# Performance work log

Hardware: AMD Instinct MI355X
Metric: run time of the kernel (lower is better)

Reference implementation:

```python
import jax, jax.numpy as jnp
import numpy as np
from jax import lax

B, L, D_MODEL = 2, 2048, 1024
D_INNER, D_STATE, DT_RANK, D_CONV = 2048, 16, 64, 4


def setup_inputs() -> dict:
    key = jax.random.key(0)
    ks = jax.random.split(key, 10)
    s = 0.02
    A_log = jnp.log(jnp.broadcast_to(jnp.arange(1, D_STATE + 1, dtype=jnp.float32), (D_INNER, D_STATE)))
    return {
        "x": jax.random.normal(ks[0], (B, L, D_MODEL), jnp.float32),
        "in_proj_w": jax.random.normal(ks[1], (2 * D_INNER, D_MODEL), jnp.float32) * s,
        "conv_w": jax.random.normal(ks[2], (D_INNER, 1, D_CONV), jnp.float32) * s,
        "conv_b": jax.random.normal(ks[3], (D_INNER,), jnp.float32) * s,
        "x_proj_w": jax.random.normal(ks[4], (DT_RANK + 2 * D_STATE, D_INNER), jnp.float32) * s,
        "dt_proj_w": jax.random.normal(ks[5], (D_INNER, DT_RANK), jnp.float32) * s,
        "dt_proj_b": jax.random.normal(ks[6], (D_INNER,), jnp.float32) * s,
        "A_log": A_log,
        "D": jnp.ones((D_INNER,), jnp.float32),
        "out_proj_w": jax.random.normal(ks[7], (D_MODEL, D_INNER), jnp.float32) * s,
    }


def _silu(v):
    return v * jax.nn.sigmoid(v)


def _mamba_forward(x, in_proj_w, conv_w, conv_b, x_proj_w, dt_proj_w, dt_proj_b, A_log, D, out_proj_w):
    b, l, _ = x.shape
    xr = jnp.einsum('bld,ed->ble', x, in_proj_w)          # (b, l, 2*d_inner)
    xs, res = jnp.split(xr, 2, axis=-1)
    # causal depthwise conv over time
    xc = jnp.transpose(xs, (0, 2, 1))                     # (b, d_inner, l)
    xc = lax.conv_general_dilated(
        xc, conv_w, window_strides=(1,), padding=[(D_CONV - 1, 0)],
        feature_group_count=D_INNER,
        dimension_numbers=('NCH', 'OIH', 'NCH')) + conv_b[None, :, None]
    u = _silu(jnp.transpose(xc, (0, 2, 1)))               # (b, l, d_inner)
    # SSM parameters
    A = -jnp.exp(A_log)                                   # (d_inner, d_state)
    x_dbl = jnp.einsum('bld,ed->ble', u, x_proj_w)        # (b, l, dt_rank + 2*d_state)
    dt, Bm, Cm = jnp.split(x_dbl, [DT_RANK, DT_RANK + D_STATE], axis=-1)
    delta = jax.nn.softplus(jnp.einsum('blr,dr->bld', dt, dt_proj_w) + dt_proj_b)
    # discretize
    deltaA = jnp.exp(jnp.einsum('bld,dn->bldn', delta, A))        # (b, l, d_inner, d_state)
    deltaBu = jnp.einsum('bld,bln,bld->bldn', delta, Bm, u)       # (b, l, d_inner, d_state)
    # sequential selective scan over time
    def step(h, inp):
        dA, dBu, c = inp
        h = dA * h + dBu                                  # (b, d_inner, d_state)
        y = jnp.einsum('bdn,bn->bd', h, c)
        return h, y
    xs_scan = (jnp.transpose(deltaA, (1, 0, 2, 3)),
               jnp.transpose(deltaBu, (1, 0, 2, 3)),
               jnp.transpose(Cm, (1, 0, 2)))
    h0 = jnp.zeros((b, D_INNER, D_STATE), u.dtype)
    _, ys = lax.scan(step, h0, xs_scan)                   # (l, b, d_inner)
    y = jnp.transpose(ys, (1, 0, 2)) + u * D              # skip connection
    y = y * _silu(res)                                    # gate
    return jnp.einsum('bld,ed->ble', y, out_proj_w)       # (b, l, d_model)


def reference(x, in_proj_w, conv_w, conv_b, x_proj_w, dt_proj_w, dt_proj_b, A_log, D, out_proj_w):
    return _mamba_forward(x, in_proj_w, conv_w, conv_b, x_proj_w, dt_proj_w, dt_proj_b, A_log, D, out_proj_w)
```

## Files before the change

### kernel.cpp

```cpp
#include <hip/hip_runtime.h>
#include <hip/hip_bf16.h>
#include <math.h>

#define B_SZ 2
#define L_SZ 2048
#define DMODEL 1024
#define DINNER 2048
#define DSTATE 16
#define DTRANK 64
#define M_ROWS (B_SZ * L_SZ)

#define CH 32
#define CLEN (L_SZ / CH)
#define CPB 64

#define KSPLIT 8
#define KC (DINNER / KSPLIT)

typedef short shortx8 __attribute__((ext_vector_type(8)));
typedef float floatx4 __attribute__((ext_vector_type(4)));
typedef float floatx16 __attribute__((ext_vector_type(16)));

__device__ __forceinline__ float softplusf(float x) {
    return fmaxf(x, 0.f) + log1pf(expf(-fabsf(x)));
}
__device__ __forceinline__ float siluf(float x) {
    return x * (1.f / (1.f + expf(-x)));
}

__device__ __forceinline__ void async_ld16(const void* g, void* l) {
    __builtin_amdgcn_global_load_lds(
        (__attribute__((address_space(1))) void*)(unsigned long long)g,
        (__attribute__((address_space(3))) void*)(unsigned int)(unsigned long long)l,
        16, 0, 0);
}


template <int LO>
__global__ __launch_bounds__(256) void split3_kernel(
    const float* __restrict__ src, unsigned short* __restrict__ dst)
{
    int i = blockIdx.x * 256 + threadIdx.x;
    int row = i & 4095;
    int k8s = i >> 12;
    const float* s = src + (size_t)row * 1024 + k8s * 8;
    float4 v0 = *(const float4*)s;
    float4 v1 = *(const float4*)(s + 4);
    float vs[8] = {v0.x, v0.y, v0.z, v0.w, v1.x, v1.y, v1.z, v1.w};
    unsigned short hsv[8], lsv[8];
#pragma unroll
    for (int j = 0; j < 8; ++j) {
        __hip_bfloat16 h = __float2bfloat16(vs[j]);
        __hip_bfloat16 l = __float2bfloat16(vs[j] - __bfloat162float(h));
        hsv[j] = *(unsigned short*)&h;
        lsv[j] = *(unsigned short*)&l;
    }
    shortx8 hv = *(shortx8*)hsv;
    shortx8 lv = *(shortx8*)lsv;
    int p = row >> 8, rr = row & 255;
    int tloc = k8s >> 3;
    int sh = (k8s >> 2) & 1;
    int k8l = k8s & 3;
    size_t unit = (size_t)(k8l * 256 + rr) * 8;
#pragma unroll
    for (int e = 0; e < 3; ++e) {
        int T = e * 16 + tloc;
        size_t off = (size_t)(p * 96 + T * 2 + sh) * 8192 + unit;
        shortx8 val = (LO == 1) ? (e == 1 ? lv : hv) : (e == 2 ? lv : hv);
        *(shortx8*)&dst[off] = val;
    }
}

template <int KT>
__global__ __launch_bounds__(512, 2) void gemm_8ph(
    const unsigned short* __restrict__ Ap,
    const unsigned short* __restrict__ Bp,
    float* __restrict__ C, int ldc)
{
    __shared__ unsigned short lds[65536];

    const int tid = threadIdx.x;
    const int lane = tid & 63;
    const int w = tid >> 6;
    const int wm = w >> 2, wn = w & 3;
    const int l15 = lane & 15, l4 = lane >> 4;

    int id = blockIdx.x;
    id = (id & 7) * 32 + (id >> 3);
    const int bm = id >> 4, bn = id & 15;

    const unsigned short* ga = Ap + (size_t)bm * KT * 16384;
    const unsigned short* gb = Bp + (size_t)bn * KT * 16384;

    const int rA = (l4 * 256 + wm * 128 + l15) * 8;
    const int rB = (l4 * 256 + wn * 64 + l15) * 8;

    floatx4 acc[8][4] = {};
    shortx8 bfr[4];

    auto STAGE = [&](int vt, int ab, int s) {
        int T = vt < KT ? vt : KT - 1;
        const unsigned short* src = (ab ? gb : ga) + ((size_t)T * 2 + s) * 8192 + tid * 8;
        unsigned short* dst = (unsigned short*)lds + (vt & 1) * 32768 + ab * 16384 + s * 8192 + tid * 8;
        async_ld16(src, dst);
        async_ld16(src + 4096, dst + 4096);
    };

#define MFMA16(MH)                                                                             \
    acc[(MH)*4+0][0] = __builtin_amdgcn_mfma_f32_16x16x32_bf16(af0, bfr[0], acc[(MH)*4+0][0], 0,0,0); \
    acc[(MH)*4+0][1] = __builtin_amdgcn_mfma_f32_16x16x32_bf16(af0, bfr[1], acc[(MH)*4+0][1], 0,0,0); \
    acc[(MH)*4+0][2] = __builtin_amdgcn_mfma_f32_16x16x32_bf16(af0, bfr[2], acc[(MH)*4+0][2], 0,0,0); \
    acc[(MH)*4+0][3] = __builtin_amdgcn_mfma_f32_16x16x32_bf16(af0, bfr[3], acc[(MH)*4+0][3], 0,0,0); \
    acc[(MH)*4+1][0] = __builtin_amdgcn_mfma_f32_16x16x32_bf16(af1, bfr[0], acc[(MH)*4+1][0], 0,0,0); \
    acc[(MH)*4+1][1] = __builtin_amdgcn_mfma_f32_16x16x32_bf16(af1, bfr[1], acc[(MH)*4+1][1], 0,0,0); \
    acc[(MH)*4+1][2] = __builtin_amdgcn_mfma_f32_16x16x32_bf16(af1, bfr[2], acc[(MH)*4+1][2], 0,0,0); \
    acc[(MH)*4+1][3] = __builtin_amdgcn_mfma_f32_16x16x32_bf16(af1, bfr[3], acc[(MH)*4+1][3], 0,0,0); \
    acc[(MH)*4+2][0] = __builtin_amdgcn_mfma_f32_16x16x32_bf16(af2, bfr[0], acc[(MH)*4+2][0], 0,0,0); \
    acc[(MH)*4+2][1] = __builtin_amdgcn_mfma_f32_16x16x32_bf16(af2, bfr[1], acc[(MH)*4+2][1], 0,0,0); \
    acc[(MH)*4+2][2] = __builtin_amdgcn_mfma_f32_16x16x32_bf16(af2, bfr[2], acc[(MH)*4+2][2], 0,0,0); \
    acc[(MH)*4+2][3] = __builtin_amdgcn_mfma_f32_16x16x32_bf16(af2, bfr[3], acc[(MH)*4+2][3], 0,0,0); \
    acc[(MH)*4+3][0] = __builtin_amdgcn_mfma_f32_16x16x32_bf16(af3, bfr[0], acc[(MH)*4+3][0], 0,0,0); \
    acc[(MH)*4+3][1] = __builtin_amdgcn_mfma_f32_16x16x32_bf16(af3, bfr[1], acc[(MH)*4+3][1], 0,0,0); \
    acc[(MH)*4+3][2] = __builtin_amdgcn_mfma_f32_16x16x32_bf16(af3, bfr[2], acc[(MH)*4+3][2], 0,0,0); \
    acc[(MH)*4+3][3] = __builtin_amdgcn_mfma_f32_16x16x32_bf16(af3, bfr[3], acc[(MH)*4+3][3], 0,0,0);

#define PHASE(SLOT, S, MH, SVT, SAB, SS, VM)                                   \
    {                                                                          \
        const unsigned short* Ab = &lds[(SLOT)*32768 + (S)*8192] + rA;         \
        shortx8 af0 = *(const shortx8*)&Ab[((MH)*4 + 0) * 128];                \
        shortx8 af1 = *(const shortx8*)&Ab[((MH)*4 + 1) * 128];                \
        shortx8 af2 = *(const shortx8*)&Ab[((MH)*4 + 2) * 128];                \
        shortx8 af3 = *(const shortx8*)&Ab[((MH)*4 + 3) * 128];                \
        if ((MH) == 0) {                                                       \
            const unsigned short* Bb = &lds[(SLOT)*32768 + 16384 + (S)*8192] + rB; \
            bfr[0] = *(const shortx8*)&Bb[0];                                  \
            bfr[1] = *(const shortx8*)&Bb[128];                                \
            bfr[2] = *(const shortx8*)&Bb[256];                                \
            bfr[3] = *(const shortx8*)&Bb[384];                                \
        }                                                                      \
        STAGE(SVT, SAB, SS);                                                   \
        __builtin_amdgcn_s_barrier();                                          \
        asm volatile("s_waitcnt lgkmcnt(0)" ::: "memory");                     \
        __builtin_amdgcn_s_setprio(1);                                         \
        MFMA16(MH)                                                             \
        __builtin_amdgcn_s_setprio(0);                                         \
        if (VM) { asm volatile("s_waitcnt vmcnt(4)" ::: "memory"); }           \
        __builtin_amdgcn_s_barrier();                                          \
    }

    STAGE(0, 0, 0); STAGE(0, 1, 0); STAGE(0, 0, 1); STAGE(0, 1, 1);
    STAGE(1, 0, 0); STAGE(1, 1, 0);
    asm volatile("s_waitcnt vmcnt(4)" ::: "memory");
    __builtin_amdgcn_s_barrier();

#pragma unroll 1
    for (int i = 0; i < KT / 2; ++i) {
        const int t2 = 2 * i;
        PHASE(0, 0, 0, t2 + 1, 0, 1, 0)
        PHASE(0, 0, 1, t2 + 1, 1, 1, 0)
        PHASE(0, 1, 0, t2 + 2, 0, 0, 0)
        PHASE(0, 1, 1, t2 + 2, 1, 0, 1)
        PHASE(1, 0, 0, t2 + 2, 0, 1, 0)
        PHASE(1, 0, 1, t2 + 2, 1, 1, 0)
        PHASE(1, 1, 0, t2 + 3, 0, 0, 0)
        PHASE(1, 1, 1, t2 + 3, 1, 0, 1)
    }

#undef PHASE
#undef MFMA16

    const int c0 = bn * 256 + wn * 64;
    const int r0 = bm * 256 + wm * 128;
#pragma unroll
    for (int fi = 0; fi < 8; ++fi) {
#pragma unroll
        for (int fj = 0; fj < 4; ++fj) {
            int col = c0 + fj * 16 + l15;
            int rowb = r0 + fi * 16 + l4 * 4;
#pragma unroll
            for (int ri = 0; ri < 4; ++ri)
                C[(size_t)(rowb + ri) * ldc + col] = acc[fi][fj][ri];
        }
    }
}

template <int BN, int KP>
__global__ __launch_bounds__(256) void gemm_bf16_nt(
    const unsigned short* __restrict__ A,
    const unsigned short* __restrict__ Bm,
    float* __restrict__ C, int ldc)
{
    constexpr int TN32 = BN / 64;
    __shared__ unsigned short As[2 * 8192];
    __shared__ unsigned short Bs[2 * BN * 64];

    const int tid = threadIdx.x;
    const int w = tid >> 6;
    const int lane = tid & 63;
    const int wm = w >> 1, wn = w & 1;
    const int m0 = blockIdx.y * 128;
    const int n0 = blockIdx.x * BN;

    const int r4 = lane >> 2;
    const int csw = (lane & 3) ^ ((r4 >> 1) & 3);
    const int gk = csw * 8;
    const int l31 = lane & 31;
    const int khalf = lane >> 5;
    const int rsw = (l31 >> 1) & 3;

    floatx16 acc[2][TN32] = {};

    for (int k0 = 0; k0 < KP; k0 += 64) {
#pragma unroll
        for (int seg = 0; seg < 2; ++seg) {
            const unsigned short* Asrc = A + seg * KP;
            const unsigned short* Bsrc = Bm + seg * KP;
#pragma unroll
            for (int t = 0; t < 2; ++t) {
#pragma unroll
                for (int jj = 0; jj < 2; ++jj) {
                    int j = w + jj * 4;
                    async_ld16(Asrc + (size_t)(m0 + j * 16 + r4) * (2 * KP) + k0 + t * 32 + gk,
                               &As[seg * 8192 + t * 4096 + j * 512]);
                }
#pragma unroll
                for (int jj = 0; jj < BN / 64; ++jj) {
                    int j = w + jj * 4;
                    async_ld16(Bsrc + (size_t)(n0 + j * 16 + r4) * (2 * KP) + k0 + t * 32 + gk,
                               &Bs[seg * BN * 64 + t * BN * 32 + j * 512]);
                }
            }
        }
        __syncthreads();

#pragma unroll
        for (int t = 0; t < 2; ++t) {
#pragma unroll
            for (int kk = 0; kk < 2; ++kk) {
                const int pos = ((kk * 2 + khalf) ^ rsw) << 3;
                shortx8 ah[2], al[2], bh[TN32], bl[TN32];
#pragma unroll
                for (int i = 0; i < 2; ++i) {
                    int row = wm * 64 + i * 32 + l31;
                    ah[i] = *(const shortx8*)&As[t * 4096 + row * 32 + pos];
                    al[i] = *(const shortx8*)&As[8192 + t * 4096 + row * 32 + pos];
                }
#pragma unroll
                for (int j = 0; j < TN32; ++j) {
                    int col = wn * (BN / 2) + j * 32 + l31;
                    bh[j] = *(const shortx8*)&Bs[t * BN * 32 + col * 32 + pos];
                    bl[j] = *(const shortx8*)&Bs[BN * 64 + t * BN * 32 + col * 32 + pos];
                }
#pragma unroll
                for (int i = 0; i < 2; ++i)
#pragma unroll
                    for (int j = 0; j < TN32; ++j) {
                        acc[i][j] = __builtin_amdgcn_mfma_f32_32x32x16_bf16(ah[i], bh[j], acc[i][j], 0, 0, 0);
                        acc[i][j] = __builtin_amdgcn_mfma_f32_32x32x16_bf16(ah[i], bl[j], acc[i][j], 0, 0, 0);
                        acc[i][j] = __builtin_amdgcn_mfma_f32_32x32x16_bf16(al[i], bh[j], acc[i][j], 0, 0, 0);
                    }
            }
        }
        __syncthreads();
    }

#pragma unroll
    for (int i = 0; i < 2; ++i) {
#pragma unroll
        for (int j = 0; j < TN32; ++j) {
            int col = n0 + wn * (BN / 2) + j * 32 + l31;
#pragma unroll
            for (int r = 0; r < 16; ++r) {
                int row = m0 + wm * 64 + i * 32 + (r & 3) + 8 * (r >> 2) + 4 * khalf;
                C[(size_t)row * ldc + col] = acc[i][j][r];
            }
        }
    }
}

__global__ __launch_bounds__(256) void split2_kernel(
    const float* __restrict__ src, unsigned short* __restrict__ dst, int K)
{
    int i = blockIdx.x * 256 + threadIdx.x;
    int m = i / K;
    int k = i - m * K;
    float a = src[i];
    __hip_bfloat16 h = __float2bfloat16(a);
    __hip_bfloat16 l = __float2bfloat16(a - __bfloat162float(h));
    unsigned short* row = dst + (size_t)m * 2 * K;
    row[k] = *(unsigned short*)&h;
    row[K + k] = *(unsigned short*)&l;
}

__global__ __launch_bounds__(256) void xproj_splitk(
    const float* __restrict__ u, const float* __restrict__ Wx,
    float* __restrict__ Cp)
{
    __shared__ float As[16][68];
    __shared__ float Bs[16][100];

    const int tid = threadIdx.x;
    const int ks = blockIdx.x;
    const int m0 = blockIdx.y * 64;
    const int tx = tid & 15;
    const int ty = tid >> 4;

    float acc[4][6] = {};

    const int arow = tid >> 2;
    const int akk = (tid & 3) * 4;

    for (int k0 = ks * KC; k0 < (ks + 1) * KC; k0 += 16) {
        {
            float4 v = *(const float4*)&u[(size_t)(m0 + arow) * DINNER + k0 + akk];
            As[akk + 0][arow] = v.x;
            As[akk + 1][arow] = v.y;
            As[akk + 2][arow] = v.z;
            As[akk + 3][arow] = v.w;
        }
        for (int idx = tid; idx < 384; idx += 256) {
            int row = idx >> 2;
            int kk = (idx & 3) * 4;
            float4 v = *(const float4*)&Wx[(size_t)row * DINNER + k0 + kk];
            Bs[kk + 0][row] = v.x;
            Bs[kk + 1][row] = v.y;
            Bs[kk + 2][row] = v.z;
            Bs[kk + 3][row] = v.w;
        }
        __syncthreads();

#pragma unroll
        for (int k = 0; k < 16; ++k) {
            float a[4], b[6];
#pragma unroll
            for (int i = 0; i < 4; ++i) a[i] = As[k][ty * 4 + i];
#pragma unroll
            for (int j = 0; j < 6; ++j) b[j] = Bs[k][tx * 6 + j];
#pragma unroll
            for (int i = 0; i < 4; ++i)
#pragma unroll
                for (int j = 0; j < 6; ++j) acc[i][j] = fmaf(a[i], b[j], acc[i][j]);
        }
        __syncthreads();
    }

    float* outp = Cp + ((size_t)ks * M_ROWS + m0) * 96;
#pragma unroll
    for (int i = 0; i < 4; ++i)
#pragma unroll
        for (int j = 0; j < 6; ++j)
            outp[(ty * 4 + i) * 96 + tx * 6 + j] = acc[i][j];
}

__global__ __launch_bounds__(256) void xproj_reduce(
    const float* __restrict__ Cp, float* __restrict__ xdbl)
{
    int i = blockIdx.x * 256 + threadIdx.x;
    float s = 0.f;
#pragma unroll
    for (int c = 0; c < KSPLIT; ++c)
        s += Cp[(size_t)c * M_ROWS * 96 + i];
    xdbl[i] = s;
}

__global__ __launch_bounds__(256) void dtproj_kernel(
    const float* __restrict__ A, const float* __restrict__ Bw,
    const float* __restrict__ bias, float* __restrict__ Cout)
{
    __shared__ float As[64][68];
    __shared__ float Bs[64][132];

    const int tid = threadIdx.x;
    const int m0 = blockIdx.y * 64;
    const int n0 = blockIdx.x * 128;
    const int tx = tid & 15;
    const int ty = tid >> 4;

    for (int idx = tid * 4; idx < 64 * 64; idx += 1024) {
        int row = idx >> 6, kk = idx & 63;
        float4 v = *(const float4*)&A[(size_t)(m0 + row) * 96 + kk];
        As[kk + 0][row] = v.x;
        As[kk + 1][row] = v.y;
        As[kk + 2][row] = v.z;
        As[kk + 3][row] = v.w;
    }
    for (int idx = tid * 4; idx < 128 * 64; idx += 1024) {
        int row = idx >> 6, kk = idx & 63;
        float4 v = *(const float4*)&Bw[(size_t)(n0 + row) * 64 + kk];
        Bs[kk + 0][row] = v.x;
        Bs[kk + 1][row] = v.y;
        Bs[kk + 2][row] = v.z;
        Bs[kk + 3][row] = v.w;
    }
    __syncthreads();

    float acc[4][8] = {};
#pragma unroll 8
    for (int k = 0; k < 64; ++k) {
        float a[4], b[8];
        *(float4*)a = *(const float4*)&As[k][ty * 4];
        *(float4*)&b[0] = *(const float4*)&Bs[k][tx * 8];
        *(float4*)&b[4] = *(const float4*)&Bs[k][tx * 8 + 4];
#pragma unroll
        for (int i = 0; i < 4; ++i)
#pragma unroll
            for (int j = 0; j < 8; ++j) acc[i][j] = fmaf(a[i], b[j], acc[i][j]);
    }

#pragma unroll
    for (int i = 0; i < 4; ++i) {
        int m = m0 + ty * 4 + i;
        float o[8];
#pragma unroll
        for (int j = 0; j < 8; ++j)
            o[j] = softplusf(acc[i][j] + bias[n0 + tx * 8 + j]);
        float* dst = &Cout[(size_t)m * DINNER + n0 + tx * 8];
        *(float4*)&dst[0] = *(float4*)&o[0];
        *(float4*)&dst[4] = *(float4*)&o[4];
    }
}

__global__ __launch_bounds__(256) void conv_silu_v4(
    const float* __restrict__ xz, const float* __restrict__ cw,
    const float* __restrict__ cb, float* __restrict__ u)
{
    int i = blockIdx.x * 256 + threadIdx.x;
    int dq = (i & 511) << 2;
    int bl = i >> 9;
    int b = bl >> 11;
    int l = bl & 2047;

    float4 W0 = *(const float4*)&cw[(dq + 0) * 4];
    float4 W1 = *(const float4*)&cw[(dq + 1) * 4];
    float4 W2 = *(const float4*)&cw[(dq + 2) * 4];
    float4 W3 = *(const float4*)&cw[(dq + 3) * 4];
    float4 acc = *(const float4*)&cb[dq];

#pragma unroll
    for (int k = 0; k < 4; ++k) {
        int ls = l + k - 3;
        if (ls >= 0) {
            float4 v = *(const float4*)&xz[((size_t)(b << 11) + ls) * 4096 + dq];
            acc.x = fmaf(v.x, ((const float*)&W0)[k], acc.x);
            acc.y = fmaf(v.y, ((const float*)&W1)[k], acc.y);
            acc.z = fmaf(v.z, ((const float*)&W2)[k], acc.z);
            acc.w = fmaf(v.w, ((const float*)&W3)[k], acc.w);
        }
    }
    float4 r = make_float4(siluf(acc.x), siluf(acc.y), siluf(acc.z), siluf(acc.w));
    *(float4*)&u[(size_t)bl * DINNER + dq] = r;
}

template <bool PASS3>
__global__ __launch_bounds__(256) void scan_chunk(
    const float* __restrict__ dbuf, const float* __restrict__ ubuf,
    const float* __restrict__ xdbl, const float* __restrict__ A_log,
    const float* __restrict__ Dv,
    float* __restrict__ Pbuf, float* __restrict__ Sbuf,
    const float* __restrict__ xz, unsigned short* __restrict__ y2)
{
    __shared__ float sd[16][CPB];
    __shared__ float su[16][CPB];
    __shared__ float sB[16][DSTATE];
    __shared__ float sC[16][DSTATE];

    const int tid = threadIdx.x;
    const int c    = blockIdx.x % CH;
    const int dblk = (blockIdx.x / CH) % (DINNER / CPB);
    const int b    = blockIdx.x / (CH * (DINNER / CPB));
    const int d0 = dblk * CPB;
    const int dg = tid >> 2;
    const int q  = tid & 3;
    const int d  = d0 + dg;
    const size_t base_bl = (size_t)b * L_SZ + (size_t)c * CLEN;

    float Ac[4], h[4];
    float sdl = 0.f;
#pragma unroll
    for (int j = 0; j < 4; ++j)
        Ac[j] = -expf(A_log[d * DSTATE + 4 * q + j]);
    const size_t psoff = (((size_t)b * CH + c) * DINNER + d0) * DSTATE + (size_t)tid * 4;
    if (PASS3) {
        float4 h0 = *(const float4*)&Sbuf[psoff];
        h[0] = h0.x; h[1] = h0.y; h[2] = h0.z; h[3] = h0.w;
    } else {
        h[0] = h[1] = h[2] = h[3] = 0.f;
    }
    const float Dd = PASS3 ? Dv[d] : 0.f;

    const int ls = tid >> 4;
    const int g4 = (tid & 15) * 4;
    const int ln = tid & 15;

    float4 r_d = *(const float4*)&dbuf[(base_bl + ls) * DINNER + d0 + g4];
    float4 r_u = *(const float4*)&ubuf[(base_bl + ls) * DINNER + d0 + g4];
    float r_B = xdbl[(base_bl + ls) * 96 + 64 + ln];
    float r_C = xdbl[(base_bl + ls) * 96 + 80 + ln];

    for (int l0 = 0; l0 < CLEN; l0 += 16) {
        __syncthreads();
        *(float4*)&sd[ls][g4] = r_d;
        *(float4*)&su[ls][g4] = r_u;
        sB[ls][ln] = r_B;
        sC[ls][ln] = r_C;
        __syncthreads();

        if (l0 + 16 < CLEN) {
            r_d = *(const float4*)&dbuf[(base_bl + l0 + 16 + ls) * DINNER + d0 + g4];
            r_u = *(const float4*)&ubuf[(base_bl + l0 + 16 + ls) * DINNER + d0 + g4];
            r_B = xdbl[(base_bl + l0 + 16 + ls) * 96 + 64 + ln];
            r_C = xdbl[(base_bl + l0 + 16 + ls) * 96 + 80 + ln];
        }

#pragma unroll
        for (int s = 0; s < 16; ++s) {
            float dl = sd[s][dg];
            float ul = su[s][dg];
            float4 Bv = *(float4*)&sB[s][4 * q];
            float dbu = dl * ul;
            float dA0 = expf(dl * Ac[0]);
            float dA1 = expf(dl * Ac[1]);
            float dA2 = expf(dl * Ac[2]);
            float dA3 = expf(dl * Ac[3]);
            h[0] = fmaf(dA0, h[0], dbu * Bv.x);
            h[1] = fmaf(dA1, h[1], dbu * Bv.y);
            h[2] = fmaf(dA2, h[2], dbu * Bv.z);
            h[3] = fmaf(dA3, h[3], dbu * Bv.w);
            if (!PASS3) {
                sdl += dl;
            } else {
                float4 Cv = *(float4*)&sC[s][4 * q];
                float y = h[0] * Cv.x + h[1] * Cv.y + h[2] * Cv.z + h[3] * Cv.w;
                y += __shfl_xor(y, 1);
                y += __shfl_xor(y, 2);
                if (q == 0) su[s][dg] = fmaf(ul, Dd, y);
            }
        }

        if (PASS3) {
            __syncthreads();
            size_t row = base_bl + l0 + ls;
            float4 yv = *(float4*)&su[ls][g4];
            float4 rv = *(const float4*)&xz[row * 4096 + 2048 + d0 + g4];
            float a0 = yv.x * siluf(rv.x);
            float a1 = yv.y * siluf(rv.y);
            float a2 = yv.z * siluf(rv.z);
            float a3 = yv.w * siluf(rv.w);
            __hip_bfloat16 h0 = __float2bfloat16(a0), h1 = __float2bfloat16(a1);
            __hip_bfloat16 h2 = __float2bfloat16(a2), h3 = __float2bfloat16(a3);
            __hip_bfloat16 l0b = __float2bfloat16(a0 - __bfloat162float(h0));
            __hip_bfloat16 l1b = __float2bfloat16(a1 - __bfloat162float(h1));
            __hip_bfloat16 l2b = __float2bfloat16(a2 - __bfloat162float(h2));
            __hip_bfloat16 l3b = __float2bfloat16(a3 - __bfloat162float(h3));
            ushort4 hv = make_ushort4(*(unsigned short*)&h0, *(unsigned short*)&h1,
                                      *(unsigned short*)&h2, *(unsigned short*)&h3);
            ushort4 lv = make_ushort4(*(unsigned short*)&l0b, *(unsigned short*)&l1b,
                                      *(unsigned short*)&l2b, *(unsigned short*)&l3b);
            unsigned short* yrow = y2 + row * 2 * DINNER + d0 + g4;
            *(ushort4*)&yrow[0] = hv;
            *(ushort4*)&yrow[DINNER] = lv;
        }
    }

    if (!PASS3) {
        *(float4*)&Pbuf[psoff] = make_float4(expf(Ac[0] * sdl), expf(Ac[1] * sdl),
                                             expf(Ac[2] * sdl), expf(Ac[3] * sdl));
        *(float4*)&Sbuf[psoff] = make_float4(h[0], h[1], h[2], h[3]);
    }
}

__global__ __launch_bounds__(256) void scan_combine(
    const float* __restrict__ Pbuf, float* __restrict__ Sbuf)
{
    int t = blockIdx.x * 256 + threadIdx.x;
    int b = t >> 15;
    int rem = t & 32767;
    size_t base = (size_t)b * CH * DINNER * DSTATE + rem;
    float H = 0.f;
#pragma unroll 4
    for (int c = 0; c < CH; ++c) {
        size_t off = base + (size_t)c * DINNER * DSTATE;
        float S = Sbuf[off];
        float P = Pbuf[off];
        Sbuf[off] = H;
        H = fmaf(P, H, S);
    }
}

extern "C" void kernel_launch(void* const* d_in, const int* in_sizes, int n_in,
                              void* d_out, int out_size, void* d_ws, size_t ws_size,
                              hipStream_t stream)
{
    const float* x          = (const float*)d_in[0];
    const float* in_proj_w  = (const float*)d_in[1];
    const float* conv_w     = (const float*)d_in[2];
    const float* conv_b     = (const float*)d_in[3];
    const float* x_proj_w   = (const float*)d_in[4];
    const float* dt_proj_w  = (const float*)d_in[5];
    const float* dt_proj_b  = (const float*)d_in[6];
    const float* A_log      = (const float*)d_in[7];
    const float* Dv         = (const float*)d_in[8];
    const float* out_proj_w = (const float*)d_in[9];
    float* out = (float*)d_out;

    char* w = (char*)d_ws;
    float* xz   = (float*)(w);
    float* u    = (float*)(w + 67108864);
    float* dbuf = (float*)(w + 100663296);
    float* xdbl = (float*)(w + 134217728);
    float* Pbuf = (float*)(w + 135790592);
    float* Sbuf = (float*)(w + 144179200);
    unsigned short* y2  = (unsigned short*)(w + 152567808);
    unsigned short* w2b = (unsigned short*)(w + 135790592);
    float* Cp = (float*)(w + 152567808);
    unsigned short* x2p  = (unsigned short*)(w + 67108864);
    unsigned short* w2ap = (unsigned short*)(w + 100663296);

    split3_kernel<1><<<2048, 256, 0, stream>>>(x, x2p);
    split3_kernel<2><<<2048, 256, 0, stream>>>(in_proj_w, w2ap);
    gemm_8ph<48><<<256, 512, 0, stream>>>(x2p, w2ap, xz, 4096);
    conv_silu_v4<<<(M_ROWS * 512) / 256, 256, 0, stream>>>(xz, conv_w, conv_b, u);
    {
        dim3 g(KSPLIT, M_ROWS / 64);
        xproj_splitk<<<g, 256, 0, stream>>>(u, x_proj_w, Cp);
        xproj_reduce<<<(M_ROWS * 96) / 256, 256, 0, stream>>>(Cp, xdbl);
    }
    {
        dim3 g(DINNER / 128, M_ROWS / 64);
        dtproj_kernel<<<g, 256, 0, stream>>>(xdbl, dt_proj_w, dt_proj_b, dbuf);
    }
    {
        const int nblk = B_SZ * (DINNER / CPB) * CH;
        scan_chunk<false><<<nblk, 256, 0, stream>>>(dbuf, u, xdbl, A_log, Dv, Pbuf, Sbuf, nullptr, nullptr);
        scan_combine<<<B_SZ * DINNER * DSTATE / 256, 256, 0, stream>>>(Pbuf, Sbuf);
        scan_chunk<true><<<nblk, 256, 0, stream>>>(dbuf, u, xdbl, A_log, Dv, nullptr, Sbuf, xz, y2);
    }
    split2_kernel<<<(DMODEL * DINNER) / 256, 256, 0, stream>>>(out_proj_w, w2b, DINNER);
    {
        dim3 g(1024 / 64, M_ROWS / 128);
        gemm_bf16_nt<64, 2048><<<g, 256, 0, stream>>>(y2, w2b, out, 1024);
    }
}
```

Before: 496.2 us.

## Route out_proj through packed 8-phase MFMA GEMM with split-K and reduction

The out-projection now uses the pipelined 8-phase bf16x3 GEMM instead of the simpler gemm_bf16_nt kernel. The scan writes y directly in the packed tile layout, and the split kernel is generalised to pack out_proj_w into the same layout. Because the output has only 16x4 tiles of 256x256, the GEMM is split 4 ways along K to fill 256 blocks, and a separate kreduce4 pass sums the partials. This adds a 64 MB partial buffer plus an extra reduction pass, in exchange for higher MFMA throughput and async-pipelined loads.

Result: slower. 517.2 us (+4.2%).

```diff
diff --git a/kernel.cpp b/kernel.cpp
--- a/kernel.cpp
+++ b/kernel.cpp
@@ -36,14 +36,15 @@
 }
 
 
-template <int LO>
+template <int ROWS, int KSRC>
 __global__ __launch_bounds__(256) void split3_kernel(
     const float* __restrict__ src, unsigned short* __restrict__ dst)
 {
+    constexpr int SEGT = KSRC / 64;
     int i = blockIdx.x * 256 + threadIdx.x;
-    int row = i & 4095;
-    int k8s = i >> 12;
-    const float* s = src + (size_t)row * 1024 + k8s * 8;
+    int row = i & (ROWS - 1);
+    int k8s = i / ROWS;
+    const float* s = src + (size_t)row * KSRC + k8s * 8;
     float4 v0 = *(const float4*)s;
     float4 v1 = *(const float4*)(s + 4);
     float vs[8] = {v0.x, v0.y, v0.z, v0.w, v1.x, v1.y, v1.z, v1.w};
@@ -55,27 +56,20 @@
         hsv[j] = *(unsigned short*)&h;
         lsv[j] = *(unsigned short*)&l;
     }
-    shortx8 hv = *(shortx8*)hsv;
-    shortx8 lv = *(shortx8*)lsv;
-    int p = row >> 8, rr = row & 255;
     int tloc = k8s >> 3;
     int sh = (k8s >> 2) & 1;
     int k8l = k8s & 3;
-    size_t unit = (size_t)(k8l * 256 + rr) * 8;
-#pragma unroll
-    for (int e = 0; e < 3; ++e) {
-        int T = e * 16 + tloc;
-        size_t off = (size_t)(p * 96 + T * 2 + sh) * 8192 + unit;
-        shortx8 val = (LO == 1) ? (e == 1 ? lv : hv) : (e == 2 ? lv : hv);
-        *(shortx8*)&dst[off] = val;
-    }
-}
-
-template <int KT>
+    size_t off = ((size_t)(row >> 8) * 4 * SEGT + tloc * 2 + sh) * 8192
+               + (size_t)(k8l * 256 + (row & 255)) * 8;
+    *(shortx8*)&dst[off] = *(shortx8*)hsv;
+    *(shortx8*)&dst[off + (size_t)2 * SEGT * 8192] = *(shortx8*)lsv;
+}
+
+template <int KT, int SEGT, int NB, int KS, int LDC>
 __global__ __launch_bounds__(512, 2) void gemm_8ph(
     const unsigned short* __restrict__ Ap,
     const unsigned short* __restrict__ Bp,
-    float* __restrict__ C, int ldc)
+    float* __restrict__ C)
 {
     __shared__ unsigned short lds[65536];
 
@@ -87,10 +81,15 @@
 
     int id = blockIdx.x;
     id = (id & 7) * 32 + (id >> 3);
-    const int bm = id >> 4, bn = id & 15;
-
-    const unsigned short* ga = Ap + (size_t)bm * KT * 16384;
-    const unsigned short* gb = Bp + (size_t)bn * KT * 16384;
+    constexpr int NBK = NB * KS;
+    const int bm = id / NBK;
+    const int rem = id % NBK;
+    const int bn = rem % NB;
+    const int ks = rem / NB;
+    const int T0 = ks * KT;
+
+    const unsigned short* ga = Ap + (size_t)bm * 4 * SEGT * 8192;
+    const unsigned short* gb = Bp + (size_t)bn * 4 * SEGT * 8192;
 
     const int rA = (l4 * 256 + wm * 128 + l15) * 8;
     const int rB = (l4 * 256 + wn * 64 + l15) * 8;
@@ -100,7 +99,10 @@
 
     auto STAGE = [&](int vt, int ab, int s) {
         int T = vt < KT ? vt : KT - 1;
-        const unsigned short* src = (ab ? gb : ga) + ((size_t)T * 2 + s) * 8192 + tid * 8;
+        int Tv = T0 + T;
+        int Tm = ab ? (Tv >= SEGT ? Tv - SEGT : Tv)
+                    : (Tv >= 2 * SEGT ? Tv - 2 * SEGT : Tv);
+        const unsigned short* src = (ab ? gb : ga) + ((size_t)Tm * 2 + s) * 8192 + tid * 8;
         unsigned short* dst = (unsigned short*)lds + (vt & 1) * 32768 + ab * 16384 + s * 8192 + tid * 8;
         async_ld16(src, dst);
         async_ld16(src + 4096, dst + 4096);
@@ -169,6 +171,7 @@
 #undef PHASE
 #undef MFMA16
 
+    float* Cb = C + (size_t)ks * ((size_t)M_ROWS * LDC);
     const int c0 = bn * 256 + wn * 64;
     const int r0 = bm * 256 + wm * 128;
 #pragma unroll
@@ -179,117 +182,22 @@
             int rowb = r0 + fi * 16 + l4 * 4;
 #pragma unroll
             for (int ri = 0; ri < 4; ++ri)
-                C[(size_t)(rowb + ri) * ldc + col] = acc[fi][fj][ri];
-        }
-    }
-}
-
-template <int BN, int KP>
-__global__ __launch_bounds__(256) void gemm_bf16_nt(
-    const unsigned short* __restrict__ A,
-    const unsigned short* __restrict__ Bm,
-    float* __restrict__ C, int ldc)
-{
-    constexpr int TN32 = BN / 64;
-    __shared__ unsigned short As[2 * 8192];
-    __shared__ unsigned short Bs[2 * BN * 64];
-
-    const int tid = threadIdx.x;
-    const int w = tid >> 6;
-    const int lane = tid & 63;
-    const int wm = w >> 1, wn = w & 1;
-    const int m0 = blockIdx.y * 128;
-    const int n0 = blockIdx.x * BN;
-
-    const int r4 = lane >> 2;
-    const int csw = (lane & 3) ^ ((r4 >> 1) & 3);
-    const int gk = csw * 8;
-    const int l31 = lane & 31;
-    const int khalf = lane >> 5;
-    const int rsw = (l31 >> 1) & 3;
-
-    floatx16 acc[2][TN32] = {};
-
-    for (int k0 = 0; k0 < KP; k0 += 64) {
-#pragma unroll
-        for (int seg = 0; seg < 2; ++seg) {
-            const unsigned short* Asrc = A + seg * KP;
-            const unsigned short* Bsrc = Bm + seg * KP;
-#pragma unroll
-            for (int t = 0; t < 2; ++t) {
-#pragma unroll
-                for (int jj = 0; jj < 2; ++jj) {
-                    int j = w + jj * 4;
-                    async_ld16(Asrc + (size_t)(m0 + j * 16 + r4) * (2 * KP) + k0 + t * 32 + gk,
-                               &As[seg * 8192 + t * 4096 + j * 512]);
-                }
-#pragma unroll
-                for (int jj = 0; jj < BN / 64; ++jj) {
-                    int j = w + jj * 4;
-                    async_ld16(Bsrc + (size_t)(n0 + j * 16 + r4) * (2 * KP) + k0 + t * 32 + gk,
-                               &Bs[seg * BN * 64 + t * BN * 32 + j * 512]);
-                }
-            }
-        }
-        __syncthreads();
-
-#pragma unroll
-        for (int t = 0; t < 2; ++t) {
-#pragma unroll
-            for (int kk = 0; kk < 2; ++kk) {
-                const int pos = ((kk * 2 + khalf) ^ rsw) << 3;
-                shortx8 ah[2], al[2], bh[TN32], bl[TN32];
-#pragma unroll
-                for (int i = 0; i < 2; ++i) {
-                    int row = wm * 64 + i * 32 + l31;
-                    ah[i] = *(const shortx8*)&As[t * 4096 + row * 32 + pos];
-                    al[i] = *(const shortx8*)&As[8192 + t * 4096 + row * 32 + pos];
-                }
-#pragma unroll
-                for (int j = 0; j < TN32; ++j) {
-                    int col = wn * (BN / 2) + j * 32 + l31;
-                    bh[j] = *(const shortx8*)&Bs[t * BN * 32 + col * 32 + pos];
-                    bl[j] = *(const shortx8*)&Bs[BN * 64 + t * BN * 32 + col * 32 + pos];
-                }
-#pragma unroll
-                for (int i = 0; i < 2; ++i)
-#pragma unroll
-                    for (int j = 0; j < TN32; ++j) {
-                        acc[i][j] = __builtin_amdgcn_mfma_f32_32x32x16_bf16(ah[i], bh[j], acc[i][j], 0, 0, 0);
-                        acc[i][j] = __builtin_amdgcn_mfma_f32_32x32x16_bf16(ah[i], bl[j], acc[i][j], 0, 0, 0);
-                        acc[i][j] = __builtin_amdgcn_mfma_f32_32x32x16_bf16(al[i], bh[j], acc[i][j], 0, 0, 0);
-                    }
-            }
-        }
-        __syncthreads();
-    }
-
-#pragma unroll
-    for (int i = 0; i < 2; ++i) {
-#pragma unroll
-        for (int j = 0; j < TN32; ++j) {
-            int col = n0 + wn * (BN / 2) + j * 32 + l31;
-#pragma unroll
-            for (int r = 0; r < 16; ++r) {
-                int row = m0 + wm * 64 + i * 32 + (r & 3) + 8 * (r >> 2) + 4 * khalf;
-                C[(size_t)row * ldc + col] = acc[i][j][r];
-            }
-        }
-    }
-}
-
-__global__ __launch_bounds__(256) void split2_kernel(
-    const float* __restrict__ src, unsigned short* __restrict__ dst, int K)
-{
-    int i = blockIdx.x * 256 + threadIdx.x;
-    int m = i / K;
-    int k = i - m * K;
-    float a = src[i];
-    __hip_bfloat16 h = __float2bfloat16(a);
-    __hip_bfloat16 l = __float2bfloat16(a - __bfloat162float(h));
-    unsigned short* row = dst + (size_t)m * 2 * K;
-    row[k] = *(unsigned short*)&h;
-    row[K + k] = *(unsigned short*)&l;
+                Cb[(size_t)(rowb + ri) * LDC + col] = acc[fi][fj][ri];
+        }
+    }
+}
+
+__global__ __launch_bounds__(256) void kreduce4(
+    const float* __restrict__ P, float* __restrict__ out)
+{
+    int i = (blockIdx.x * 256 + threadIdx.x) * 4;
+    float4 a = *(const float4*)&P[i];
+    float4 b = *(const float4*)&P[i + 4194304];
+    float4 c = *(const float4*)&P[i + 8388608];
+    float4 d = *(const float4*)&P[i + 12582912];
+    float4 r = make_float4(a.x + b.x + c.x + d.x, a.y + b.y + c.y + d.y,
+                           a.z + b.z + c.z + d.z, a.w + b.w + c.w + d.w);
+    *(float4*)&out[i] = r;
 }
 
 __global__ __launch_bounds__(256) void xproj_splitk(
@@ -496,6 +404,10 @@
     float4 r_u = *(const float4*)&ubuf[(base_bl + ls) * DINNER + d0 + g4];
     float r_B = xdbl[(base_bl + ls) * 96 + 64 + ln];
     float r_C = xdbl[(base_bl + ls) * 96 + 80 + ln];
+
+    const int krow = d0 + g4;
+    const int tloc = krow >> 6, sh5 = (krow >> 5) & 1;
+    const int k8l = (krow >> 3) & 3, jj = krow & 7;
 
     for (int l0 = 0; l0 < CLEN; l0 += 16) {
         __syncthreads();
@@ -556,9 +468,10 @@
                                       *(unsigned short*)&h2, *(unsigned short*)&h3);
             ushort4 lv = make_ushort4(*(unsigned short*)&l0b, *(unsigned short*)&l1b,
                                       *(unsigned short*)&l2b, *(unsigned short*)&l3b);
-            unsigned short* yrow = y2 + row * 2 * DINNER + d0 + g4;
-            *(ushort4*)&yrow[0] = hv;
-            *(ushort4*)&yrow[DINNER] = lv;
+            size_t offh = ((size_t)(row >> 8) * 128 + tloc * 2 + sh5) * 8192
+                        + (size_t)(k8l * 256 + (int)(row & 255)) * 8 + jj;
+            *(ushort4*)&y2[offh] = hv;
+            *(ushort4*)&y2[offh + 524288] = lv;
         }
     }
 
@@ -610,15 +523,16 @@
     float* xdbl = (float*)(w + 134217728);
     float* Pbuf = (float*)(w + 135790592);
     float* Sbuf = (float*)(w + 144179200);
-    unsigned short* y2  = (unsigned short*)(w + 152567808);
-    unsigned short* w2b = (unsigned short*)(w + 135790592);
-    float* Cp = (float*)(w + 152567808);
+    unsigned short* y2p = (unsigned short*)(w + 152567808);
+    float* Cp  = (float*)(w + 152567808);
+    unsigned short* w2bp = (unsigned short*)(w + 135790592);
+    float* Cp2 = (float*)(w);
     unsigned short* x2p  = (unsigned short*)(w + 67108864);
     unsigned short* w2ap = (unsigned short*)(w + 100663296);
 
-    split3_kernel<1><<<2048, 256, 0, stream>>>(x, x2p);
-    split3_kernel<2><<<2048, 256, 0, stream>>>(in_proj_w, w2ap);
-    gemm_8ph<48><<<256, 512, 0, stream>>>(x2p, w2ap, xz, 4096);
+    split3_kernel<4096, 1024><<<2048, 256, 0, stream>>>(x, x2p);
+    split3_kernel<4096, 1024><<<2048, 256, 0, stream>>>(in_proj_w, w2ap);
+    gemm_8ph<48, 16, 16, 1, 4096><<<256, 512, 0, stream>>>(x2p, w2ap, xz);
     conv_silu_v4<<<(M_ROWS * 512) / 256, 256, 0, stream>>>(xz, conv_w, conv_b, u);
     {
         dim3 g(KSPLIT, M_ROWS / 64);
@@ -633,11 +547,9 @@
         const int nblk = B_SZ * (DINNER / CPB) * CH;
         scan_chunk<false><<<nblk, 256, 0, stream>>>(dbuf, u, xdbl, A_log, Dv, Pbuf, Sbuf, nullptr, nullptr);
         scan_combine<<<B_SZ * DINNER * DSTATE / 256, 256, 0, stream>>>(Pbuf, Sbuf);
-        scan_chunk<true><<<nblk, 256, 0, stream>>>(dbuf, u, xdbl, A_log, Dv, nullptr, Sbuf, xz, y2);
-    }
-    split2_kernel<<<(DMODEL * DINNER) / 256, 256, 0, stream>>>(out_proj_w, w2b, DINNER);
-    {
-        dim3 g(1024 / 64, M_ROWS / 128);
-        gemm_bf16_nt<64, 2048><<<g, 256, 0, stream>>>(y2, w2b, out, 1024);
-    }
-}
+        split3_kernel<1024, 2048><<<1024, 256, 0, stream>>>(out_proj_w, w2bp);
+        scan_chunk<true><<<nblk, 256, 0, stream>>>(dbuf, u, xdbl, A_log, Dv, nullptr, Sbuf, xz, y2p);
+    }
+    gemm_8ph<24, 32, 4, 4, 1024><<<256, 512, 0, stream>>>(y2p, w2bp, Cp2);
+    kreduce4<<<(M_ROWS * DMODEL) / 1024, 256, 0, stream>>>(Cp2, out);
+}
```
